# Optimization experiments

Measured on AMD Instinct MI355X. Metric: run time of the kernel, lower is better.

Reference implementation:

```python
import jax, jax.numpy as jnp
import numpy as np

K = 2  # k-MIS hops (matches init k)


def _khop_min(mr, row, col, n, k):
    # k rounds of: min over in-neighbors (scatter_min row->col), then min with self
    for _ in range(k):
        neigh = jax.ops.segment_min(mr[row], col, num_segments=n)
        mr = jnp.minimum(mr, neigh)
    return mr


def _score_and_rank(x, lin_w, lin_b, row, col, n, k):
    score = jax.nn.sigmoid(x @ lin_w + lin_b)  # [n,1] linear scorer
    s = score[:, 0]
    # 'greedy' heuristic: s' = s / ((A+I)^k 1)
    ks = jnp.ones_like(s)
    for _ in range(k):
        ks = ks + jax.ops.segment_sum(ks[row], col, num_segments=n)
    upd = s / ks
    perm = jnp.argsort(-upd)  # descending: higher score -> lower rank
    rank = jnp.zeros(n, jnp.int32).at[perm].set(jnp.arange(n, dtype=jnp.int32))
    return score, rank


def _kmis_cluster(row, col, rank, n, k):
    nI = jnp.int32(n)

    def cond(state):
        return ~jnp.all(state[1])

    def body(state):
        mis, mask, mr = state
        mr = _khop_min(mr, row, col, n, k)
        mis = mis | (rank == mr)
        m = mis.astype(jnp.int32)
        for _ in range(k):  # propagate coverage k hops (scatter_max)
            neigh = jax.ops.segment_max(m[row], col, num_segments=n)
            m = jnp.maximum(m, jnp.clip(neigh, 0, 1))
        mask = m > 0
        mr = jnp.where(mask, nI, rank)
        return mis, mask, mr

    mis0 = jnp.zeros(n, bool)
    mis, _, _ = jax.lax.while_loop(cond, body, (mis0, mis0, rank))
    # clustering: propagate min rank of MIS nodes k hops
    mr = _khop_min(jnp.where(mis, rank, nI), row, col, n, k)
    mis_idx = jnp.nonzero(mis)[0]  # eager (data-dependent size, like torch)
    rank_mis = rank[mis_idx]
    order = jnp.argsort(rank_mis)
    # unique(min_rank).inverse then perm[clusters] == index into MIS nodes (node order)
    cluster = order[jnp.searchsorted(rank_mis[order], mr)]
    return mis_idx, cluster


def setup_inputs() -> dict:
    key = jax.random.key(0)
    k1, k2, k3, _ = jax.random.split(key, 4)
    n, e, d = 100000, 1600000, 256
    x = jax.random.normal(k1, (n, d), jnp.float32)
    edge_index = jax.random.randint(k2, (2, e), 0, n, jnp.int32)
    lin_w = jax.random.normal(k3, (d, 1), jnp.float32) * 0.05
    lin_b = jnp.zeros((1,), jnp.float32)
    return {"x": x, "edge_index": edge_index, "lin_w": lin_w, "lin_b": lin_b}


def reference(x, edge_index, lin_w, lin_b):
    n = x.shape[0]
    row, col = edge_index[0], edge_index[1]
    score, rank = _score_and_rank(x, lin_w, lin_b, row, col, n, K)
    mis_idx, cluster = _kmis_cluster(row, col, rank, n, K)
    # pool edges: relabel endpoints, coalesce duplicates with 'sum', drop self-loops
    pairs = jnp.stack([cluster[row], cluster[col]], axis=1)
    uniq, inv = jnp.unique(pairs, axis=0, return_inverse=True)
    val = jax.ops.segment_sum(jnp.ones(row.shape[0], jnp.float32), inv.reshape(-1), num_segments=uniq.shape[0])
    keep = uniq[:, 0] != uniq[:, 1]
    new_edge_index = uniq[keep].T
    new_edge_attr = val[keep]
    # pool nodes: score_passthrough='before', aggr_x=None -> select MIS rows
    x_pool = (x * score)[mis_idx]
    return x_pool, new_edge_index, new_edge_attr
```

## Files before the change

### kernel.cpp

```cpp
#include <hip/hip_runtime.h>
#include <math.h>

#define BLOCK 256
#define EGRID 2048
#define SG    512
#define NTHE (EGRID*BLOCK)
#define NWVE (NTHE/64)
#define INF_ 0x7fffffff
#define TB   6000
#define AWMAX 224
#define TBCAP 7168
#define DENSE_ITERS 6

struct KParams {
  const float* x;
  const int*   ei;
  const float* w;
  const float* bb;
  float* out;
  int n, e, d, out_size;
  int* ws;
  long long ws_ints;
};

struct Lay {
  float* score; int *ks1,*cursor;
  int *keyA,*idxA,*keyB,*idxB,*lrank;
  int *rank,*mr,*t1,*mis,*mm,*misPre,*r2c,*clus,*colPtr,*rowPtr;
  unsigned *bh,*dtot,*dbase,*btot,*bbase;
  int *cnts,*colSrc,*rowDst,*pairCnt;
  long long unionBase;
};

__device__ __host__ inline Lay mklay(int* ws, int n, int e) {
  Lay L;
  L.score=(float*)ws;
  L.ks1   = ws + (size_t)1*n;
  L.cursor= ws + (size_t)2*n;
  L.keyA  = ws + (size_t)3*n;
  L.idxA  = ws + (size_t)4*n;
  L.keyB  = ws + (size_t)5*n;
  L.idxB  = ws + (size_t)6*n;
  L.lrank = ws + (size_t)7*n;
  L.rank  = ws + (size_t)8*n;
  L.mr    = ws + (size_t)9*n;
  L.t1    = ws + (size_t)10*n;
  L.mis   = ws + (size_t)11*n;
  L.mm    = ws + (size_t)12*n;
  L.misPre= ws + (size_t)13*n;
  L.r2c   = ws + (size_t)14*n;
  L.clus  = ws + (size_t)15*n;
  L.colPtr= ws + (size_t)16*n;
  L.rowPtr= ws + (size_t)17*n + 64;
  int* sm = ws + (size_t)18*n + 128;
  L.bh    = (unsigned*)sm;
  L.dtot  = L.bh + 256*SG;
  L.dbase = L.dtot + 256;
  L.btot  = L.dbase + 256;
  L.bbase = L.btot + SG;
  L.cnts  = (int*)(L.bbase + SG);
  L.unionBase = 18ll*n + 128 + 256ll*SG + 512 + 2ll*SG + 16;
  L.colSrc  = ws + L.unionBase;
  L.rowDst  = L.colSrc + e;
  L.pairCnt = ws + L.unionBase;
  return L;
}

__device__ inline int gmin_(const int* __restrict__ s, const int* __restrict__ val,
                            int p, int pe, int m) {
  for (; p+3 < pe; p += 4) {
    int a0=s[p],a1=s[p+1],a2=s[p+2],a3=s[p+3];
    int t0=val[a0],t1=val[a1],t2=val[a2],t3=val[a3];
    t0=min(t0,t1); t2=min(t2,t3); t0=min(t0,t2); if (t0<m) m=t0;
  }
  for (; p<pe; ++p){ int t=val[s[p]]; if (t<m) m=t; }
  return m;
}
__device__ inline int gor_(const int* __restrict__ s, const int* __restrict__ val,
                           int p, int pe, int m) {
  for (; p+3 < pe; p += 4) m |= val[s[p]] | val[s[p+1]] | val[s[p+2]] | val[s[p+3]];
  for (; p<pe; ++p) m |= val[s[p]];
  return m;
}
__device__ inline int gsum_(const int* __restrict__ s, const int* __restrict__ val,
                            int p, int pe, int m) {
  for (; p+3 < pe; p += 4) m += val[s[p]] + val[s[p+1]] + val[s[p+2]] + val[s[p+3]];
  for (; p<pe; ++p) m += val[s[p]];
  return m;
}

__device__ inline int btotPrefix(const unsigned* btot, int upto) {
  __shared__ int red[256];
  int tid = threadIdx.x;
  int partial = 0;
  for (int idx = tid; idx < upto; idx += 256) partial += (int)btot[idx];
  __syncthreads();
  red[tid] = partial; __syncthreads();
  for (int off = 128; off > 0; off >>= 1) { if (tid < off) red[tid] += red[tid+off]; __syncthreads(); }
  int r = red[0]; __syncthreads();
  return r;
}

__global__ __launch_bounds__(BLOCK) void k_score(KParams P) {
  Lay L = mklay(P.ws, P.n, P.e);
  int gid = blockIdx.x*BLOCK + threadIdx.x;
  int lane = gid & 63, gwv = gid >> 6;
  int d4 = P.d >> 2;
  double bconst = (double)P.bb[0];
  const float4* w4 = (const float4*)P.w;
  for (int v = gwv; v < P.n; v += NWVE) {
    const float4* xr = (const float4*)(P.x + (size_t)v*P.d);
    double s = 0.0;
    for (int q = lane; q < d4; q += 64) {
      float4 xv = xr[q], wv = w4[q];
      s += (double)xv.x*wv.x + (double)xv.y*wv.y + (double)xv.z*wv.z + (double)xv.w*wv.w;
    }
    for (int off = 32; off > 0; off >>= 1) s += __shfl_down(s, off);
    if (lane == 0) L.score[v] = (float)(1.0/(1.0+exp(-(s+bconst))));
  }
  for (int v = gid; v < P.n; v += NTHE) L.ks1[v] = 0;
}

__global__ __launch_bounds__(BLOCK) void k_degree(KParams P) {
  Lay L = mklay(P.ws, P.n, P.e);
  const int* col = P.ei + P.e;
  int gid = blockIdx.x*BLOCK + threadIdx.x;
  for (int j = gid; j < P.e; j += NTHE) atomicAdd(&L.ks1[col[j]], 1);
}

__global__ __launch_bounds__(BLOCK) void k_scan1(KParams P) {
  Lay L = mklay(P.ws, P.n, P.e);
  __shared__ int lds[256];
  int tid = threadIdx.x, bid = blockIdx.x;
  int chunk = (P.n + SG - 1)/SG;
  int ig = bid*chunk + tid;
  bool valid = (tid < chunk) && (ig < P.n);
  int v2 = valid ? L.ks1[ig] : 0;
  lds[tid] = v2; __syncthreads();
  for (int off = 1; off < 256; off <<= 1) {
    int t = (tid >= off) ? lds[tid-off] : 0; __syncthreads();
    lds[tid] += t; __syncthreads();
  }
  if (valid) L.colPtr[ig] = lds[tid] - v2;
  if (tid == 0) L.btot[bid] = (unsigned)lds[255];
}

__global__ __launch_bounds__(BLOCK) void k_scan3(KParams P) {
  Lay L = mklay(P.ws, P.n, P.e);
  int tid = threadIdx.x, bid = blockIdx.x;
  int base = btotPrefix(L.btot, bid);
  int chunk = (P.n + SG - 1)/SG;
  int ig = bid*chunk + tid;
  if (tid < chunk && ig < P.n) {
    int cp = L.colPtr[ig] + base;
    L.colPtr[ig] = cp; L.cursor[ig] = cp; L.ks1[ig] += 1;
  }
  if (bid == 0 && tid == 0) L.colPtr[P.n] = P.e;
}

__global__ __launch_bounds__(BLOCK) void k_csr(KParams P) {
  Lay L = mklay(P.ws, P.n, P.e);
  const int* __restrict__ row = P.ei; const int* __restrict__ col = P.ei + P.e;
  int grp = blockIdx.x & 7;
  int bwg = blockIdx.x >> 3;
  int nbw = gridDim.x >> 3;
  int lo = (int)((long long)grp * P.n >> 3);
  int hi = (int)((long long)(grp+1) * P.n >> 3);
  int gid = bwg*BLOCK + threadIdx.x;
  int stride = nbw*BLOCK;
  for (int j = gid; j < P.e; j += stride) {
    int c = col[j];
    if (c >= lo && c < hi) {
      int pos = atomicAdd(&L.cursor[c], 1);
      L.colSrc[pos] = row[j];
    }
  }
}

__global__ __launch_bounds__(BLOCK) void k_keygen(KParams P) {
  Lay L = mklay(P.ws, P.n, P.e);
  int v = blockIdx.x*BLOCK + threadIdx.x;
  if (v >= P.n) return;
  int s = gsum_(L.colSrc, L.ks1, L.colPtr[v], L.colPtr[v+1], L.ks1[v]);
  float upd = L.score[v] / (float)s;
  unsigned u = __float_as_uint(upd);
  u = (u & 0x80000000u) ? (~u) : (u | 0x80000000u);
  ((unsigned*)L.keyA)[v] = ~u;
  ((unsigned*)L.idxA)[v] = (unsigned)v;
}

__global__ __launch_bounds__(BLOCK) void k_sort_local(KParams P, int pass) {
  Lay L = mklay(P.ws, P.n, P.e);
  __shared__ int ldsH[1024];
  int tid = threadIdx.x, bid = blockIdx.x, lane = tid & 63, wib = tid >> 6;
  unsigned* sk = (pass & 1) ? (unsigned*)L.keyB : (unsigned*)L.keyA;
  int shift = pass*8;
  for (int i = tid; i < 1024; i += BLOCK) ldsH[i] = 0;
  __syncthreads();
  int chunk = (P.n + SG - 1)/SG;
  int ig = bid*chunk + tid;
  bool valid = (tid < chunk) && (ig < P.n);
  int dig = 0;
  if (valid) dig = (int)((sk[ig] >> shift) & 255u);
  unsigned long long mmask = __ballot(valid);
  for (int b = 0; b < 8; ++b) {
    unsigned long long bm = __ballot((dig >> b) & 1);
    mmask &= ((dig >> b) & 1) ? bm : ~bm;
  }
  int lp = 0;
  if (valid) {
    lp = __popcll(mmask & ((1ull << lane) - 1ull));
    if (lp == 0) ldsH[wib*256 + dig] = __popcll(mmask);
  }
  __syncthreads();
  if (tid < 256) {
    int c0=ldsH[tid], c1=ldsH[256+tid], c2=ldsH[512+tid], c3=ldsH[768+tid];
    ldsH[tid]=0; ldsH[256+tid]=c0; ldsH[512+tid]=c0+c1; ldsH[768+tid]=c0+c1+c2;
    L.bh[(size_t)tid*SG + bid] = (unsigned)(c0+c1+c2+c3);
  }
  __syncthreads();
  if (valid) ((unsigned*)L.lrank)[ig] = (unsigned)(ldsH[wib*256 + dig] + lp);
}

__global__ __launch_bounds__(BLOCK) void k_sort_scan1(KParams P) {
  Lay L = mklay(P.ws, P.n, P.e);
  int g = blockIdx.x*BLOCK + threadIdx.x;
  int dg = g >> 6, lane = g & 63;
  if (dg >= 256) return;
  unsigned running = 0;
  for (int r = 0; r < SG/64; ++r) {
    unsigned v = L.bh[(size_t)dg*SG + r*64 + lane];
    unsigned incl = v;
    for (int off = 1; off < 64; off <<= 1) { unsigned t = __shfl_up(incl, off); if (lane >= off) incl += t; }
    L.bh[(size_t)dg*SG + r*64 + lane] = incl - v + running;
    running += __shfl(incl, 63);
  }
  if (lane == 0) L.dtot[dg] = running;
}

__global__ __launch_bounds__(BLOCK) void k_sort_scatter(KParams P, int pass) {
  Lay L = mklay(P.ws, P.n, P.e);
  __shared__ unsigned sdb[256];
  unsigned *sk,*si,*dk,*di;
  if (pass & 1) { sk=(unsigned*)L.keyB; si=(unsigned*)L.idxB; dk=(unsigned*)L.keyA; di=(unsigned*)L.idxA; }
  else          { sk=(unsigned*)L.keyA; si=(unsigned*)L.idxA; dk=(unsigned*)L.keyB; di=(unsigned*)L.idxB; }
  int tid = threadIdx.x, bid = blockIdx.x;
  unsigned myv = L.dtot[tid];
  sdb[tid] = myv; __syncthreads();
  for (int off = 1; off < 256; off <<= 1) {
    unsigned t = (tid >= off) ? sdb[tid-off] : 0u; __syncthreads();
    sdb[tid] += t; __syncthreads();
  }
  unsigned excl = sdb[tid] - myv; __syncthreads();
  sdb[tid] = excl; __syncthreads();
  int chunk = (P.n + SG - 1)/SG;
  int ig = bid*chunk + tid;
  if (tid < chunk && ig < P.n) {
    unsigned key = sk[ig];
    int dig = (int)((key >> (pass*8)) & 255u);
    unsigned pos = sdb[dig] + L.bh[(size_t)dig*SG + bid] + ((unsigned*)L.lrank)[ig];
    dk[pos] = key; di[pos] = si[ig];
  }
}

__global__ __launch_bounds__(BLOCK) void k_rankinit(KParams P) {
  Lay L = mklay(P.ws, P.n, P.e);
  int i = blockIdx.x*BLOCK + threadIdx.x;
  if (blockIdx.x == 0 && threadIdx.x == 0) {
    L.cnts[4] = P.n;
    L.cnts[5] = 0;
  }
  if (i >= P.n) return;
  int v = (int)((unsigned*)L.idxA)[i];
  L.rank[v] = i;
  L.mm[v] = i;
  L.mis[v] = 0;
}

__global__ __launch_bounds__(BLOCK) void k_dmin(KParams P, int t) {
  Lay L = mklay(P.ws, P.n, P.e);
  if (L.cnts[4+(t&1)] <= TB) return;
  int w = blockIdx.x*BLOCK + threadIdx.x;
  if (w >= P.n) return;
  L.mr[w] = gmin_(L.colSrc, L.mm, L.colPtr[w], L.colPtr[w+1], L.mm[w]);
}
__global__ __launch_bounds__(BLOCK) void k_dsel(KParams P, int t) {
  Lay L = mklay(P.ws, P.n, P.e);
  int q = t & 1;
  int A = L.cnts[4+q];
  if (A <= TB) return;
  int i = blockIdx.x*BLOCK + threadIdx.x;
  if (i >= A) return;
  int v = (t == 0) ? i : (q ? L.keyB : L.keyA)[i];
  int m2 = gmin_(L.colSrc, L.mr, L.colPtr[v], L.colPtr[v+1], L.mr[v]);
  if (L.rank[v] == m2) L.mis[v] = 1;
}
__global__ __launch_bounds__(BLOCK) void k_dor(KParams P, int t) {
  Lay L = mklay(P.ws, P.n, P.e);
  int q = t & 1;
  if (L.cnts[4+q] <= TB) return;
  int w = blockIdx.x*BLOCK + threadIdx.x;
  if (blockIdx.x == 0 && threadIdx.x == 0) L.cnts[4+(1-q)] = 0;
  if (w >= P.n) return;
  L.t1[w] = gor_(L.colSrc, L.mis, L.colPtr[w], L.colPtr[w+1], L.mis[w]);
}
__global__ __launch_bounds__(BLOCK) void k_drb(KParams P, int t) {
  Lay L = mklay(P.ws, P.n, P.e);
  int q = t & 1;
  int A = L.cnts[4+q];
  int* act  = (t == 0) ? (int*)0 : (q ? L.keyB : L.keyA);
  int* nact = q ? L.keyA : L.keyB;
  int gid = blockIdx.x*BLOCK + threadIdx.x;
  if (A <= TB) {
    for (int i = gid; i < A; i += (P.n + BLOCK - 1)/BLOCK*BLOCK) nact[i] = act[i];
    if (gid == 0) L.cnts[4+(1-q)] = A;
    return;
  }
  int lane = threadIdx.x & 63;
  bool aliveF = false; int v = 0;
  if (gid < A) {
    v = (t == 0) ? gid : act[gid];
    int dead = gor_(L.colSrc, L.t1, L.colPtr[v], L.colPtr[v+1], L.t1[v]);
    if (dead) L.mm[v] = INF_; else aliveF = true;
  }
  unsigned long long mk = __ballot(aliveF);
  int cntw = __popcll(mk);
  if (cntw) {
    int fl = __ffsll((unsigned long long)mk) - 1;
    int base = 0;
    if (lane == fl) base = atomicAdd(&L.cnts[4+(1-q)], cntw);
    base = __shfl(base, fl);
    if (aliveF) nact[base + __popcll(mk & ((1ull<<lane)-1ull))] = v;
  }
}

__global__ __launch_bounds__(BLOCK) void k_tcomp1(KParams P) {
  Lay L = mklay(P.ws, P.n, P.e);
  __shared__ int lds[256];
  int tid = threadIdx.x, bid = blockIdx.x;
  int chunk = (P.n + SG - 1)/SG;
  int ig = bid*chunk + tid;
  bool valid = (tid < chunk) && (ig < P.n);
  int f = 0;
  if (valid) { int v = (int)((unsigned*)L.idxA)[ig]; f = (L.mm[v] != INF_) ? 1 : 0; }
  lds[tid] = f; __syncthreads();
  for (int off = 1; off < 256; off <<= 1) {
    int t = (tid >= off) ? lds[tid-off] : 0; __syncthreads();
    lds[tid] += t; __syncthreads();
  }
  if (valid) L.t1[ig] = lds[tid] - f;
  if (tid == 0) L.btot[bid] = (unsigned)lds[255];
}
__global__ __launch_bounds__(BLOCK) void k_tcomp3(KParams P) {
  Lay L = mklay(P.ws, P.n, P.e);
  int tid = threadIdx.x, bid = blockIdx.x;
  int base = btotPrefix(L.btot, bid);
  int chunk = (P.n + SG - 1)/SG;
  int ig = bid*chunk + tid;
  if (tid < chunk && ig < P.n) {
    int v = (int)((unsigned*)L.idxA)[ig];
    if (L.mm[v] != INF_) {
      int pos = L.t1[ig] + base;
      L.lrank[pos] = v;
      L.cursor[v] = pos;
    } else L.cursor[v] = -1;
  }
  int A = L.cnts[4];
  if (A > 0) {
    int AW = (A + 31) >> 5;
    int AWP = (AW + 3) & ~3;
    unsigned* bs = (unsigned*)L.rowDst;
    long long tot = (long long)A * AWP;
    for (long long idx = (long long)bid*BLOCK + tid; idx < tot; idx += (long long)SG*BLOCK) bs[idx] = 0u;
    bool transOk = (L.unionBase + 2ll*P.e + tot <= P.ws_ints);
    if (transOk) {
      unsigned* tr = (unsigned*)(P.ws + L.unionBase + 2ll*P.e);
      for (long long idx = (long long)bid*BLOCK + tid; idx < tot; idx += (long long)SG*BLOCK) tr[idx] = 0u;
    }
  }
}
__global__ __launch_bounds__(BLOCK) void k_tbuild(KParams P) {
  Lay L = mklay(P.ws, P.n, P.e);
  int A = L.cnts[4];
  if (A <= 0) return;
  int AW = (A + 31) >> 5;
  int AWP = (AW + 3) & ~3;
  unsigned* bs = (unsigned*)L.rowDst;
  bool transOk = (L.unionBase + 2ll*P.e + (long long)A*AWP <= P.ws_ints);
  unsigned* tr = transOk ? (unsigned*)(P.ws + L.unionBase + 2ll*P.e) : (unsigned*)0;
  const int* __restrict__ cp = L.colPtr;
  const int* __restrict__ cs = L.colSrc;
  const int* __restrict__ nodeIdx = L.cursor;
  int gid = blockIdx.x*BLOCK + threadIdx.x;
  int lane = gid & 63, gwv = gid >> 6;
  int nW = (gridDim.x*BLOCK) >> 6;
  for (int i = gwv; i < A; i += nW) {
    int v = L.lrank[i];
    unsigned* row = bs + (size_t)i*AWP;
    unsigned ibit = 1u << (i & 31);
    int iw = i >> 5;
    if (lane == 0) {
      atomicOr(&row[iw], ibit);
      if (tr) atomicOr(&tr[(size_t)i*AWP + iw], ibit);
    }
    int p0 = cp[v], p1 = cp[v+1];
    for (int p = p0 + lane; p < p1; p += 64) {
      int u = cs[p];
      int j = nodeIdx[u];
      if (j >= 0) {
        atomicOr(&row[j >> 5], 1u << (j & 31));
        if (tr) atomicOr(&tr[(size_t)j*AWP + iw], ibit);
      }
      int p3 = cp[u+1];
      for (int p2 = cp[u]; p2 < p3; ++p2) {
        int w2 = cs[p2];
        int j2 = nodeIdx[w2];
        if (j2 >= 0) {
          atomicOr(&row[j2 >> 5], 1u << (j2 & 31));
          if (tr) atomicOr(&tr[(size_t)j2*AWP + iw], ibit);
        }
      }
    }
  }
}
__global__ __launch_bounds__(1024) void k_trounds(KParams P) {
  Lay L = mklay(P.ws, P.n, P.e);
  __shared__ __align__(16) unsigned aliveW[AWMAX];
  __shared__ __align__(16) unsigned selW[AWMAX];
  __shared__ __align__(16) unsigned deadW[AWMAX];
  __shared__ int selList[TBCAP];
  __shared__ unsigned char pw[TBCAP];
  __shared__ int scnt, selCnt;
  int A = L.cnts[4];
  if (A <= 0) return;
  int AW = (A + 31) >> 5;
  int AWP = (AW + 3) & ~3;
  const unsigned* __restrict__ bs = (const unsigned*)L.rowDst;
  bool transOk = (L.unionBase + 2ll*P.e + (long long)A*AWP <= P.ws_ints);
  const unsigned* __restrict__ tr = (const unsigned*)(P.ws + L.unionBase + 2ll*P.e);
  const int* __restrict__ S = L.lrank;
  const uint4* __restrict__ a4 = (const uint4*)aliveW;
  int tid = threadIdx.x;
  for (int w = tid; w < AWP; w += 1024) {
    int base = w*32; int c = A - base;
    aliveW[w] = (c >= 32) ? 0xffffffffu : ((c > 0) ? ((1u << c) - 1u) : 0u);
  }
  for (int i = tid; i < A; i += 1024) pw[i] = 0;
  __syncthreads();
  for (int rounds = 0; rounds < 8192; ++rounds) {
    for (int w = tid; w < AWP; w += 1024) { selW[w] = 0u; deadW[w] = 0u; }
    if (tid == 0) { scnt = 0; selCnt = 0; }
    __syncthreads();
    for (int i = tid; i < A; i += 1024) {
      if ((aliveW[i>>5] >> (i&31)) & 1u) {
        const unsigned* __restrict__ row = bs + (size_t)i*AWP;
        const uint4* __restrict__ r4 = (const uint4*)row;
        int wl = i >> 5;
        int nf = wl >> 2;
        int g = (int)pw[i];
        unsigned any = 0;
        for (; g + 2 <= nf; g += 2) {
          uint4 a = r4[g],   b = r4[g+1];
          uint4 av = a4[g],  bv = a4[g+1];
          unsigned r0 = (a.x&av.x)|(a.y&av.y)|(a.z&av.z)|(a.w&av.w);
          unsigned r1 = (b.x&bv.x)|(b.y&bv.y)|(b.z&bv.z)|(b.w&bv.w);
          if (r0 | r1) { any = 1; if (!r0) ++g; break; }
        }
        if (!any && g < nf) {
          uint4 a = r4[g]; uint4 av = a4[g];
          unsigned r0 = (a.x&av.x)|(a.y&av.y)|(a.z&av.z)|(a.w&av.w);
          if (r0) any = 1; else ++g;
        }
        pw[i] = (unsigned char)g;
        if (!any) {
          for (int w2 = nf << 2; w2 < wl; ++w2) any |= row[w2] & aliveW[w2];
          if (!any && (i & 31)) any = row[wl] & aliveW[wl] & ((1u << (i&31)) - 1u);
        }
        if (!any) {
          int sp = atomicAdd(&selCnt, 1);
          selList[sp] = i;
          atomicOr(&selW[i>>5], 1u << (i&31));
          L.mis[S[i]] = 1;
        }
      }
    }
    __syncthreads();
    int nsel = selCnt;
    if (nsel == 0) break;
    int surv = 0;
    if (transOk) {
      int w = tid & 255, qs = tid >> 8;
      if (w < AW) {
        unsigned acc = 0;
        for (int q = qs; q < nsel; q += 4) acc |= tr[(size_t)selList[q]*AWP + w];
        if (acc) atomicOr(&deadW[w], acc);
      }
      __syncthreads();
      for (int w2 = tid; w2 < AW; w2 += 1024) {
        unsigned na = aliveW[w2] & ~deadW[w2];
        aliveW[w2] = na;
        surv += __popc(na);
      }
    } else {
      for (int i = tid; i < A; i += 1024) {
        if ((aliveW[i>>5] >> (i&31)) & 1u) {
          const uint4* __restrict__ r4 = (const uint4*)(bs + (size_t)i*AWP);
          const uint4* __restrict__ s4 = (const uint4*)selW;
          unsigned dead = 0;
          int ng = AWP >> 2;
          for (int g2 = 0; g2 < ng; ++g2) {
            uint4 a = r4[g2], sa = s4[g2];
            dead |= (a.x&sa.x)|(a.y&sa.y)|(a.z&sa.z)|(a.w&sa.w);
          }
          if (dead) atomicAnd(&aliveW[i>>5], ~(1u << (i&31)));
          else ++surv;
        }
      }
    }
    if (surv) atomicAdd(&scnt, surv);
    __syncthreads();
    int sc = scnt;
    __syncthreads();
    if (sc == 0) break;
  }
}

__global__ __launch_bounds__(BLOCK) void k_scanM1(KParams P) {
  Lay L = mklay(P.ws, P.n, P.e);
  __shared__ int lds[256];
  int tid = threadIdx.x, bid = blockIdx.x;
  int chunk = (P.n + SG - 1)/SG;
  int ig = bid*chunk + tid;
  bool valid = (tid < chunk) && (ig < P.n);
  int v2 = 0;
  if (valid) {
    v2 = L.mis[ig];
    L.mm[ig] = v2 ? L.rank[ig] : P.n;
  }
  lds[tid] = v2; __syncthreads();
  for (int off = 1; off < 256; off <<= 1) {
    int t = (tid >= off) ? lds[tid-off] : 0; __syncthreads();
    lds[tid] += t; __syncthreads();
  }
  if (valid) L.misPre[ig] = lds[tid] - v2;
  if (tid == 0) L.btot[bid] = (unsigned)lds[255];
}
__global__ __launch_bounds__(BLOCK) void k_fin1(KParams P) {
  Lay L = mklay(P.ws, P.n, P.e);
  int v = blockIdx.x*BLOCK + threadIdx.x;
  if (v >= P.n) return;
  L.t1[v] = gmin_(L.colSrc, L.mm, L.colPtr[v], L.colPtr[v+1], L.mm[v]);
}
__global__ __launch_bounds__(BLOCK) void k_fin2(KParams P) {
  Lay L = mklay(P.ws, P.n, P.e);
  int v = blockIdx.x*BLOCK + threadIdx.x;
  if (v >= P.n) return;
  L.mr[v] = gmin_(L.colSrc, L.t1, L.colPtr[v], L.colPtr[v+1], L.t1[v]);
}
__global__ __launch_bounds__(BLOCK) void k_scanM3(KParams P) {
  Lay L = mklay(P.ws, P.n, P.e);
  int tid = threadIdx.x, bid = blockIdx.x;
  int base = btotPrefix(L.btot, bid);
  int total = btotPrefix(L.btot, SG);
  int chunk = (P.n + SG - 1)/SG;
  int ig = bid*chunk + tid;
  if (tid < chunk && ig < P.n) {
    int p = L.misPre[ig] + base;
    L.misPre[ig] = p;
    if (L.mis[ig]) L.r2c[L.rank[ig]] = p;
  }
  if (bid == 0 && tid == 0) L.cnts[2] = total;
}

__global__ __launch_bounds__(BLOCK) void k_clus(KParams P) {
  Lay L = mklay(P.ws, P.n, P.e);
  int gid = blockIdx.x*BLOCK + threadIdx.x;
  int M = L.cnts[2];
  long long M2 = (long long)M*M;
  for (int v = gid; v < P.n; v += NTHE) {
    int r3 = L.mr[v];
    L.clus[v] = (r3 >= 0 && r3 < P.n) ? L.r2c[r3] : 0;
  }
  bool pairOk = (M > 0) && (M2 < 0x7fffffffll) && (L.unionBase + M2 <= P.ws_ints);
  if (pairOk) {
    int m2i = (int)M2;
    for (int i = gid; i < m2i; i += NTHE) L.pairCnt[i] = 0;
  }
}

__global__ __launch_bounds__(BLOCK) void k_pair(KParams P) {
  Lay L = mklay(P.ws, P.n, P.e);
  int M = L.cnts[2];
  long long M2 = (long long)M*M;
  bool pairOk = (M > 0) && (M2 < 0x7fffffffll) && (L.unionBase + M2 <= P.ws_ints);
  if (!pairOk) return;
  const int* row = P.ei; const int* col = P.ei + P.e;
  int gid = blockIdx.x*BLOCK + threadIdx.x;
  for (int j = gid; j < P.e; j += NTHE) {
    int a = L.clus[row[j]], b2 = L.clus[col[j]];
    atomicAdd(&L.pairCnt[a*M + b2], 1);
  }
}

__global__ __launch_bounds__(BLOCK) void k_keep1(KParams P) {
  Lay L = mklay(P.ws, P.n, P.e);
  __shared__ int lds[256];
  int tid = threadIdx.x, bid = blockIdx.x;
  int M = L.cnts[2];
  long long M2 = (long long)M*M;
  bool pairOk = (M > 0) && (M2 < 0x7fffffffll) && (L.unionBase + M2 <= P.ws_ints);
  int m2i = pairOk ? (int)M2 : 0;
  int chunkP = pairOk ? (m2i + SG - 1)/SG : 0;
  int pstart = bid*chunkP; if (pstart > m2i) pstart = m2i;
  int pend = pstart + chunkP; if (pend > m2i) pend = m2i;
  int localKeep = 0;
  for (int i = pstart + tid; i < pend; i += BLOCK) {
    int c = L.pairCnt[i];
    if (c > 0 && (i / M) != (i % M)) ++localKeep;
  }
  lds[tid] = localKeep; __syncthreads();
  for (int off = 128; off > 0; off >>= 1) { if (tid < off) lds[tid] += lds[tid+off]; __syncthreads(); }
  if (tid == 0) L.btot[bid] = (unsigned)lds[0];
}

__global__ __launch_bounds__(BLOCK) void k_edges(KParams P) {
  Lay L = mklay(P.ws, P.n, P.e);
  __shared__ int lds[256];
  int tid = threadIdx.x, bid = blockIdx.x;
  int M = L.cnts[2];
  long long M2 = (long long)M*M;
  bool pairOk = (M > 0) && (M2 < 0x7fffffffll) && (L.unionBase + M2 <= P.ws_ints);
  if (!pairOk) return;
  int base = btotPrefix(L.btot, bid);
  int EK = btotPrefix(L.btot, SG);
  int m2i = (int)M2;
  int chunkP = (m2i + SG - 1)/SG;
  int pstart = bid*chunkP; if (pstart > m2i) pstart = m2i;
  int pend = pstart + chunkP; if (pend > m2i) pend = m2i;
  size_t eBase = (size_t)M * (size_t)P.d;
  bool outOk = (eBase + 3ull*(size_t)EK <= (size_t)P.out_size);
  int running2 = base;
  for (int t0 = pstart; t0 < pend; t0 += BLOCK) {
    int i = t0 + tid;
    int c = 0, kept = 0, a = 0, b2 = 0;
    if (i < pend) {
      c = L.pairCnt[i];
      a = i / M; b2 = i % M;
      kept = (c > 0 && a != b2) ? 1 : 0;
    }
    lds[tid] = kept; __syncthreads();
    for (int off = 1; off < 256; off <<= 1) {
      int t = (tid >= off) ? lds[tid-off] : 0; __syncthreads();
      lds[tid] += t; __syncthreads();
    }
    int incl = lds[tid], tot = lds[255];
    if (kept && outOk) {
      int j2 = running2 + incl - 1;
      P.out[eBase + (size_t)j2] = (float)a;
      P.out[eBase + (size_t)EK + (size_t)j2] = (float)b2;
      P.out[eBase + 2ull*(size_t)EK + (size_t)j2] = (float)c;
    }
    running2 += tot;
    __syncthreads();
  }
}

__global__ __launch_bounds__(BLOCK) void k_xpool(KParams P) {
  Lay L = mklay(P.ws, P.n, P.e);
  int gid = blockIdx.x*BLOCK + threadIdx.x;
  int lane = gid & 63, gwv = gid >> 6;
  int M = L.cnts[2];
  int d4 = P.d >> 2;
  size_t eBase = (size_t)M * (size_t)P.d;
  if (eBase > (size_t)P.out_size) return;
  for (int v = gwv; v < P.n; v += NWVE) {
    if (L.mis[v]) {
      int p = L.misPre[v];
      float sc = L.score[v];
      const float4* xr = (const float4*)(P.x + (size_t)v*P.d);
      float4* outr = (float4*)P.out + (size_t)p*d4;
      for (int q = lane; q < d4; q += 64) {
        float4 xv = xr[q];
        outr[q] = make_float4(xv.x*sc, xv.y*sc, xv.z*sc, xv.w*sc);
      }
    }
  }
}

extern "C" void kernel_launch(void* const* d_in, const int* in_sizes, int n_in,
                              void* d_out, int out_size, void* d_ws, size_t ws_size,
                              hipStream_t stream) {
  KParams P;
  P.x  = (const float*)d_in[0];
  P.ei = (const int*)d_in[1];
  P.w  = (const float*)d_in[2];
  P.bb = (const float*)d_in[3];
  P.out = (float*)d_out;
  P.d = in_sizes[2];
  P.n = in_sizes[0] / P.d;
  P.e = in_sizes[1] / 2;
  P.out_size = out_size;
  P.ws = (int*)d_ws;
  P.ws_ints = (long long)(ws_size / 4);
  const int nblk = (P.n + BLOCK - 1) / BLOCK;

  k_score <<<EGRID, BLOCK, 0, stream>>>(P);
  k_degree<<<EGRID, BLOCK, 0, stream>>>(P);
  k_scan1 <<<SG,    BLOCK, 0, stream>>>(P);
  k_scan3 <<<SG,    BLOCK, 0, stream>>>(P);
  k_csr   <<<EGRID, BLOCK, 0, stream>>>(P);
  k_keygen<<<nblk,  BLOCK, 0, stream>>>(P);
  for (int pass = 0; pass < 4; ++pass) {
    k_sort_local  <<<SG, BLOCK, 0, stream>>>(P, pass);
    k_sort_scan1  <<<64, BLOCK, 0, stream>>>(P);
    k_sort_scatter<<<SG, BLOCK, 0, stream>>>(P, pass);
  }
  k_rankinit<<<nblk, BLOCK, 0, stream>>>(P);
  for (int t = 0; t < DENSE_ITERS; ++t) {
    k_dmin <<<nblk, BLOCK, 0, stream>>>(P, t);
    k_dsel <<<nblk, BLOCK, 0, stream>>>(P, t);
    k_dor  <<<nblk, BLOCK, 0, stream>>>(P, t);
    k_drb  <<<nblk, BLOCK, 0, stream>>>(P, t);
  }
  k_tcomp1 <<<SG,   BLOCK, 0, stream>>>(P);
  k_tcomp3 <<<SG,   BLOCK, 0, stream>>>(P);
  k_tbuild <<<nblk, BLOCK, 0, stream>>>(P);
  k_trounds<<<1,    1024,  0, stream>>>(P);
  k_scanM1<<<SG, BLOCK, 0, stream>>>(P);
  k_fin1  <<<nblk, BLOCK, 0, stream>>>(P);
  k_fin2  <<<nblk, BLOCK, 0, stream>>>(P);
  k_scanM3<<<SG, BLOCK, 0, stream>>>(P);
  k_clus <<<EGRID, BLOCK, 0, stream>>>(P);
  k_pair <<<EGRID, BLOCK, 0, stream>>>(P);
  k_keep1<<<SG,    BLOCK, 0, stream>>>(P);
  k_edges<<<SG,    BLOCK, 0, stream>>>(P);
  k_xpool<<<EGRID, BLOCK, 0, stream>>>(P);
}
```

Measured before the change: 815.5 us.

## Track per-node alive higher-priority neighbor counts instead of rescanning bitsets each round

Adds a parallel kernel that counts, for each remaining node, how many lower-index neighbors it has in the bit matrix. The single-block round loop then selects nodes whose count is zero and, for each newly dead node, decrements the counts of its higher-index neighbors through the transposed matrix. This replaces the per-round scan of each alive node's row against the alive bitset, which is serial work inside one workgroup. In exchange it adds an extra launch, dead-list bookkeeping and many LDS atomics, and it reuses the idxB buffer as count storage.

```diff
diff --git a/kernel.cpp b/kernel.cpp
--- a/kernel.cpp
+++ b/kernel.cpp
@@ -423,14 +423,41 @@
     }
   }
 }
+__global__ __launch_bounds__(BLOCK) void k_tcnt(KParams P) {
+  Lay L = mklay(P.ws, P.n, P.e);
+  int A = L.cnts[4];
+  if (A <= 0) return;
+  int AW = (A + 31) >> 5;
+  int AWP = (AW + 3) & ~3;
+  bool transOk = (L.unionBase + 2ll*P.e + (long long)A*AWP <= P.ws_ints);
+  if (!transOk) return;
+  const unsigned* __restrict__ bs = (const unsigned*)L.rowDst;
+  int* __restrict__ cnt = L.idxB;
+  int gid = blockIdx.x*BLOCK + threadIdx.x;
+  int lane = gid & 63, gwv = gid >> 6;
+  int nW = (gridDim.x*BLOCK) >> 6;
+  for (int i = gwv; i < A; i += nW) {
+    const unsigned* __restrict__ row = bs + (size_t)i*AWP;
+    int wl = i >> 5, ib = i & 31;
+    int c = 0;
+    for (int w = lane; w <= wl; w += 64) {
+      unsigned m = row[w];
+      if (w == wl) m &= (ib ? ((1u << ib) - 1u) : 0u);
+      c += __popc(m);
+    }
+    for (int off = 32; off > 0; off >>= 1) c += __shfl_down(c, off);
+    if (lane == 0) cnt[i] = c;
+  }
+}
 __global__ __launch_bounds__(1024) void k_trounds(KParams P) {
   Lay L = mklay(P.ws, P.n, P.e);
   __shared__ __align__(16) unsigned aliveW[AWMAX];
   __shared__ __align__(16) unsigned selW[AWMAX];
   __shared__ __align__(16) unsigned deadW[AWMAX];
   __shared__ int selList[TBCAP];
-  __shared__ unsigned char pw[TBCAP];
-  __shared__ int scnt, selCnt;
+  __shared__ int deadList[TBCAP];
+  __shared__ int cntS[TBCAP];
+  __shared__ int scnt, selCnt, deadCnt;
   int A = L.cnts[4];
   if (A <= 0) return;
   int AW = (A + 31) >> 5;
@@ -439,69 +466,107 @@
   bool transOk = (L.unionBase + 2ll*P.e + (long long)A*AWP <= P.ws_ints);
   const unsigned* __restrict__ tr = (const unsigned*)(P.ws + L.unionBase + 2ll*P.e);
   const int* __restrict__ S = L.lrank;
-  const uint4* __restrict__ a4 = (const uint4*)aliveW;
   int tid = threadIdx.x;
   for (int w = tid; w < AWP; w += 1024) {
     int base = w*32; int c = A - base;
     aliveW[w] = (c >= 32) ? 0xffffffffu : ((c > 0) ? ((1u << c) - 1u) : 0u);
   }
-  for (int i = tid; i < A; i += 1024) pw[i] = 0;
-  __syncthreads();
-  for (int rounds = 0; rounds < 8192; ++rounds) {
-    for (int w = tid; w < AWP; w += 1024) { selW[w] = 0u; deadW[w] = 0u; }
-    if (tid == 0) { scnt = 0; selCnt = 0; }
+  if (transOk) {
+    const int* __restrict__ cntG = L.idxB;
+    for (int i = tid; i < A; i += 1024) cntS[i] = cntG[i];
     __syncthreads();
-    for (int i = tid; i < A; i += 1024) {
-      if ((aliveW[i>>5] >> (i&31)) & 1u) {
-        const unsigned* __restrict__ row = bs + (size_t)i*AWP;
-        const uint4* __restrict__ r4 = (const uint4*)row;
-        int wl = i >> 5;
-        int nf = wl >> 2;
-        int g = (int)pw[i];
-        unsigned any = 0;
-        for (; g + 2 <= nf; g += 2) {
-          uint4 a = r4[g],   b = r4[g+1];
-          uint4 av = a4[g],  bv = a4[g+1];
-          unsigned r0 = (a.x&av.x)|(a.y&av.y)|(a.z&av.z)|(a.w&av.w);
-          unsigned r1 = (b.x&bv.x)|(b.y&bv.y)|(b.z&bv.z)|(b.w&bv.w);
-          if (r0 | r1) { any = 1; if (!r0) ++g; break; }
-        }
-        if (!any && g < nf) {
-          uint4 a = r4[g]; uint4 av = a4[g];
-          unsigned r0 = (a.x&av.x)|(a.y&av.y)|(a.z&av.z)|(a.w&av.w);
-          if (r0) any = 1; else ++g;
-        }
-        pw[i] = (unsigned char)g;
-        if (!any) {
-          for (int w2 = nf << 2; w2 < wl; ++w2) any |= row[w2] & aliveW[w2];
-          if (!any && (i & 31)) any = row[wl] & aliveW[wl] & ((1u << (i&31)) - 1u);
-        }
-        if (!any) {
+    int wid = tid >> 6, lane = tid & 63;
+    for (int rounds = 0; rounds < 8192; ++rounds) {
+      for (int w = tid; w < AW; w += 1024) deadW[w] = 0u;
+      if (tid == 0) { scnt = 0; selCnt = 0; deadCnt = 0; }
+      __syncthreads();
+      for (int i = tid; i < A; i += 1024) {
+        if (((aliveW[i>>5] >> (i&31)) & 1u) && cntS[i] == 0) {
           int sp = atomicAdd(&selCnt, 1);
           selList[sp] = i;
-          atomicOr(&selW[i>>5], 1u << (i&31));
           L.mis[S[i]] = 1;
         }
       }
-    }
-    __syncthreads();
-    int nsel = selCnt;
-    if (nsel == 0) break;
-    int surv = 0;
-    if (transOk) {
-      int w = tid & 255, qs = tid >> 8;
-      if (w < AW) {
-        unsigned acc = 0;
-        for (int q = qs; q < nsel; q += 4) acc |= tr[(size_t)selList[q]*AWP + w];
-        if (acc) atomicOr(&deadW[w], acc);
+      __syncthreads();
+      int nsel = selCnt;
+      if (nsel == 0) break;
+      {
+        int w = tid & 255, qs = tid >> 8;
+        if (w < AW) {
+          unsigned acc = 0;
+          for (int q = qs; q < nsel; q += 4) acc |= tr[(size_t)selList[q]*AWP + w];
+          if (acc) atomicOr(&deadW[w], acc);
+        }
       }
       __syncthreads();
-      for (int w2 = tid; w2 < AW; w2 += 1024) {
-        unsigned na = aliveW[w2] & ~deadW[w2];
-        aliveW[w2] = na;
+      int surv = 0;
+      for (int w = tid; w < AW; w += 1024) {
+        unsigned dn = aliveW[w] & deadW[w];
+        unsigned na = aliveW[w] & ~deadW[w];
+        aliveW[w] = na;
         surv += __popc(na);
+        while (dn) {
+          int b = __ffs(dn) - 1; dn &= dn - 1;
+          int dp = atomicAdd(&deadCnt, 1);
+          deadList[dp] = w*32 + b;
+        }
       }
-    } else {
+      if (surv) atomicAdd(&scnt, surv);
+      __syncthreads();
+      int nd = deadCnt, sc = scnt;
+      for (int q = wid; q < nd; q += 16) {
+        int k = deadList[q];
+        const unsigned* __restrict__ trow = tr + (size_t)k*AWP;
+        int kw = k >> 5, kb = k & 31;
+        for (int w = lane; w < AW; w += 64) {
+          if (w < kw) continue;
+          unsigned m = trow[w];
+          if (w == kw) m &= (kb == 31) ? 0u : (~0u << (kb + 1));
+          while (m) {
+            int b = __ffs(m) - 1; m &= m - 1;
+            atomicSub(&cntS[w*32 + b], 1);
+          }
+        }
+      }
+      __syncthreads();
+      if (sc == 0) break;
+    }
+  } else {
+    const uint4* __restrict__ a4 = (const uint4*)aliveW;
+    __syncthreads();
+    for (int rounds = 0; rounds < 8192; ++rounds) {
+      for (int w = tid; w < AWP; w += 1024) { selW[w] = 0u; }
+      if (tid == 0) scnt = 0;
+      __syncthreads();
+      for (int i = tid; i < A; i += 1024) {
+        if ((aliveW[i>>5] >> (i&31)) & 1u) {
+          const unsigned* __restrict__ row = bs + (size_t)i*AWP;
+          const uint4* __restrict__ r4 = (const uint4*)row;
+          int wl = i >> 5;
+          int nf = wl >> 2;
+          unsigned any = 0;
+          int g = 0;
+          for (; g + 2 <= nf; g += 2) {
+            uint4 a = r4[g],   b = r4[g+1];
+            uint4 av = a4[g],  bv = a4[g+1];
+            unsigned r0 = (a.x&av.x)|(a.y&av.y)|(a.z&av.z)|(a.w&av.w);
+            unsigned r1 = (b.x&bv.x)|(b.y&bv.y)|(b.z&bv.z)|(b.w&bv.w);
+            any = r0 | r1;
+            if (any) break;
+          }
+          if (!any && g < nf) {
+            uint4 a = r4[g]; uint4 av = a4[g];
+            any = (a.x&av.x)|(a.y&av.y)|(a.z&av.z)|(a.w&av.w);
+          }
+          if (!any) {
+            for (int w2 = nf << 2; w2 < wl; ++w2) any |= row[w2] & aliveW[w2];
+            if (!any && (i & 31)) any = row[wl] & aliveW[wl] & ((1u << (i&31)) - 1u);
+          }
+          if (!any) { atomicOr(&selW[i>>5], 1u << (i&31)); L.mis[S[i]] = 1; }
+        }
+      }
+      __syncthreads();
+      int surv = 0;
       for (int i = tid; i < A; i += 1024) {
         if ((aliveW[i>>5] >> (i&31)) & 1u) {
           const uint4* __restrict__ r4 = (const uint4*)(bs + (size_t)i*AWP);
@@ -516,12 +581,12 @@
           else ++surv;
         }
       }
-    }
-    if (surv) atomicAdd(&scnt, surv);
-    __syncthreads();
-    int sc = scnt;
-    __syncthreads();
-    if (sc == 0) break;
+      if (surv) atomicAdd(&scnt, surv);
+      __syncthreads();
+      int sc = scnt;
+      __syncthreads();
+      if (sc == 0) break;
+    }
   }
 }
 
@@ -725,6 +790,7 @@
   k_tcomp1 <<<SG,   BLOCK, 0, stream>>>(P);
   k_tcomp3 <<<SG,   BLOCK, 0, stream>>>(P);
   k_tbuild <<<nblk, BLOCK, 0, stream>>>(P);
+  k_tcnt   <<<nblk, BLOCK, 0, stream>>>(P);
   k_trounds<<<1,    1024,  0, stream>>>(P);
   k_scanM1<<<SG, BLOCK, 0, stream>>>(P);
   k_fin1  <<<nblk, BLOCK, 0, stream>>>(P);
```

Result: slower. 1.024 ms (+25.6%).
